# Kernel optimization log

Hardware: AMD Instinct MI355X
Metric: run time of the kernel (lower is better)

The kernel has to match this reference:

```python
import jax, jax.numpy as jnp
import numpy as np

B, T, C, H = 2, 2048, 1024, 16
HD = C // H  # head dim = 64


def setup_inputs() -> dict:
    key = jax.random.key(0)
    ks = jax.random.split(key, 5)
    s = 1.0 / np.sqrt(C)
    return {
        "x": jax.random.normal(ks[0], (B, T, C), dtype=jnp.float32),
        "Wq": jax.random.normal(ks[1], (C, C), dtype=jnp.float32) * s,
        "bq": jnp.zeros((C,), dtype=jnp.float32),
        "Wk": jax.random.normal(ks[2], (C, C), dtype=jnp.float32) * s,
        "bk": jnp.zeros((C,), dtype=jnp.float32),
        "Wv": jax.random.normal(ks[3], (C, C), dtype=jnp.float32) * s,
        "bv": jnp.zeros((C,), dtype=jnp.float32),
        "Wp": jax.random.normal(ks[4], (C, C), dtype=jnp.float32) * s,
        "bp": jnp.zeros((C,), dtype=jnp.float32),
    }


def reference(x, Wq, bq, Wk, bk, Wv, bv, Wp, bp):
    # QKV projections -> [B, H, T, HD]
    def proj(W, b):
        return (x @ W.T + b).reshape(B, T, H, HD).transpose(0, 2, 1, 3)

    q = proj(Wq, bq)
    k = proj(Wk, bk)
    v = proj(Wv, bv)

    scale = 1.0 / np.sqrt(HD)
    att = jnp.einsum("bhtd,bhsd->bhts", q, k) * scale  # [B,H,T,T]
    causal = jnp.tril(jnp.ones((T, T), dtype=bool))
    att = jnp.where(causal, att, -jnp.inf)
    att = jax.nn.softmax(att, axis=-1)
    y = jnp.einsum("bhts,bhsd->bhtd", att, v)          # [B,H,T,HD]
    y = y.transpose(0, 2, 1, 3).reshape(B, T, C)
    return y @ Wp.T + bp
```

## Files before the change

### kernel.cpp

```cpp
#include <hip/hip_runtime.h>
#include <hip/hip_bf16.h>

#define BB 2
#define TT 2048
#define CC 1024
#define HH 16
#define HDD 64

typedef __attribute__((ext_vector_type(8))) short bf16x8;
typedef __attribute__((ext_vector_type(4))) float f32x4;

static __device__ __forceinline__ unsigned short f2bf(float f) {
  union { float f; unsigned u; } v; v.f = f;
  unsigned r = v.u + 0x7fffu + ((v.u >> 16) & 1u);
  return (unsigned short)(r >> 16);
}

static __device__ __forceinline__ unsigned fbits(float f) {
  union { float f; unsigned u; } v; v.f = f; return v.u;
}

static __device__ __forceinline__ unsigned pk_trunc(float lo, float hi) {
  return __builtin_amdgcn_perm(fbits(hi), fbits(lo), 0x07060302u);
}

static __device__ __forceinline__ void gload_lds16(const unsigned short* g, unsigned short* l) {
  __builtin_amdgcn_global_load_lds((const __attribute__((address_space(1))) void*)g,
                                   (__attribute__((address_space(3))) void*)l, 16, 0, 0);
}

__global__ __launch_bounds__(256) void convert_all(
    const float* __restrict__ x, const float* __restrict__ Wq,
    const float* __restrict__ Wk, const float* __restrict__ Wv,
    const float* __restrict__ Wp, unsigned short* __restrict__ dst)
{
  const size_t M4 = 4194304, M1 = 1048576;
  const size_t e = ((size_t)blockIdx.x * 256 + threadIdx.x) * 8;
  const float* src; size_t off;
  if (e < M4)            { src = x;  off = e; }
  else if (e < M4 + M1)  { src = Wq; off = e - M4; }
  else if (e < M4 + 2*M1){ src = Wk; off = e - M4 - M1; }
  else if (e < M4 + 3*M1){ src = Wv; off = e - M4 - 2*M1; }
  else                   { src = Wp; off = e - M4 - 3*M1; }
  float4 a = *(const float4*)(src + off);
  float4 c = *(const float4*)(src + off + 4);
  unsigned short buf[8] = {f2bf(a.x), f2bf(a.y), f2bf(a.z), f2bf(a.w),
                           f2bf(c.x), f2bf(c.y), f2bf(c.z), f2bf(c.w)};
  *(uint4*)(dst + e) = *(const uint4*)buf;
}

__global__ __launch_bounds__(256) void gemm_mfma(
    const unsigned short* __restrict__ A, const unsigned short* __restrict__ W,
    const float* __restrict__ b0, const float* __restrict__ b1, const float* __restrict__ b2,
    unsigned short* __restrict__ oQ, unsigned short* __restrict__ oK,
    unsigned short* __restrict__ oVt)
{
  __shared__ unsigned short As[128][32];
  __shared__ unsigned short Bs[128][32];
  const int t = threadIdx.x;
  const int wv = __builtin_amdgcn_readfirstlane(t >> 6);
  const int ln = t & 63;
  const int l16 = ln & 15;
  const int quad = ln >> 4;
  const int mBase = blockIdx.x * 128;
  const int nBase = blockIdx.y * 128;
  const int wm = (wv >> 1) * 64, wn = (wv & 1) * 64;

  f32x4 acc[4][4];
#pragma unroll
  for (int i = 0; i < 4; i++)
#pragma unroll
    for (int j = 0; j < 4; j++) acc[i][j] = (f32x4){0.f, 0.f, 0.f, 0.f};

  const int ca = wv * 64 + ln;
  const int cb = ca + 256;
  const int ra = ca >> 2, colA = (ca & 3) * 8;
  const int rb = cb >> 2, colB = (cb & 3) * 8;
  unsigned short* ldsA0 = &As[0][0] + (size_t)(wv * 64) * 8;
  unsigned short* ldsA1 = &As[0][0] + (size_t)(256 + wv * 64) * 8;
  unsigned short* ldsB0 = &Bs[0][0] + (size_t)(wv * 64) * 8;
  unsigned short* ldsB1 = &Bs[0][0] + (size_t)(256 + wv * 64) * 8;
  const unsigned short* apA0 = A + (size_t)(mBase + ra) * CC + colA;
  const unsigned short* apA1 = A + (size_t)(mBase + rb) * CC + colB;
  const unsigned short* apB0 = W + (size_t)(nBase + ra) * CC + colA;
  const unsigned short* apB1 = W + (size_t)(nBase + rb) * CC + colB;

  for (int kb = 0; kb < CC; kb += 32) {
    __syncthreads();
    gload_lds16(apA0 + kb, ldsA0);
    gload_lds16(apA1 + kb, ldsA1);
    gload_lds16(apB0 + kb, ldsB0);
    gload_lds16(apB1 + kb, ldsB1);
    __syncthreads();
    bf16x8 af[4], bfr[4];
#pragma unroll
    for (int i = 0; i < 4; i++) af[i] = *(const bf16x8*)&As[wm + i * 16 + l16][quad * 8];
#pragma unroll
    for (int j = 0; j < 4; j++) bfr[j] = *(const bf16x8*)&Bs[wn + j * 16 + l16][quad * 8];
#pragma unroll
    for (int i = 0; i < 4; i++)
#pragma unroll
      for (int j = 0; j < 4; j++)
        acc[i][j] = __builtin_amdgcn_mfma_f32_16x16x32_bf16(af[i], bfr[j], acc[i][j], 0, 0, 0);
  }

  const int which = nBase >> 10;
  const float* bias = which == 0 ? b0 : (which == 1 ? b1 : b2);
  unsigned short* dst = which == 0 ? oQ : (which == 1 ? oK : oVt);
  const float scl = which == 0 ? 0.1803368801f : 1.0f;
#pragma unroll
  for (int i = 0; i < 4; i++)
#pragma unroll
    for (int r = 0; r < 4; r++) {
      const int m = mBase + wm + i * 16 + quad * 4 + r;
      const int b = m >> 11, tp = m & 2047;
#pragma unroll
      for (int j = 0; j < 4; j++) {
        const int n = nBase + wn + j * 16 + l16;
        const int nl = n & 1023, h = nl >> 6, d = nl & 63;
        const unsigned short v = f2bf((acc[i][j][r] + bias[nl]) * scl);
        if (which < 2) dst[((size_t)(b * HH + h) * TT + tp) * HDD + d] = v;
        else           dst[((size_t)(b * HH + h) * HDD + d) * TT + tp] = v;
      }
    }
}

__global__ __launch_bounds__(512) void gemm_proj(
    const unsigned short* __restrict__ A, const unsigned short* __restrict__ W,
    const float* __restrict__ bias, float* __restrict__ out)
{
  __shared__ unsigned short As[128][32];
  __shared__ unsigned short Bs[128][32];
  const int t = threadIdx.x;
  const int wv = __builtin_amdgcn_readfirstlane(t >> 6);
  const int ln = t & 63;
  const int l16 = ln & 15;
  const int quad = ln >> 4;
  const int mBase = blockIdx.x * 128;
  const int nBase = blockIdx.y * 128;
  const int wm = (wv >> 2) * 64;
  const int wn = (wv & 3) * 32;

  f32x4 acc[4][2];
#pragma unroll
  for (int i = 0; i < 4; i++)
#pragma unroll
    for (int j = 0; j < 2; j++) acc[i][j] = (f32x4){0.f, 0.f, 0.f, 0.f};

  const int rs = t >> 2, cs = (t & 3) * 8;
  unsigned short* ldsA = &As[0][0] + (size_t)t * 8;
  unsigned short* ldsB = &Bs[0][0] + (size_t)t * 8;
  const unsigned short* apA = A + (size_t)(mBase + rs) * CC + cs;
  const unsigned short* apB = W + (size_t)(nBase + rs) * CC + cs;

  for (int kb = 0; kb < CC; kb += 32) {
    __syncthreads();
    gload_lds16(apA + kb, ldsA);
    gload_lds16(apB + kb, ldsB);
    __syncthreads();
    bf16x8 af[4], bfr[2];
#pragma unroll
    for (int i = 0; i < 4; i++) af[i] = *(const bf16x8*)&As[wm + i * 16 + l16][quad * 8];
#pragma unroll
    for (int j = 0; j < 2; j++) bfr[j] = *(const bf16x8*)&Bs[wn + j * 16 + l16][quad * 8];
#pragma unroll
    for (int i = 0; i < 4; i++)
#pragma unroll
      for (int j = 0; j < 2; j++)
        acc[i][j] = __builtin_amdgcn_mfma_f32_16x16x32_bf16(af[i], bfr[j], acc[i][j], 0, 0, 0);
  }

#pragma unroll
  for (int i = 0; i < 4; i++)
#pragma unroll
    for (int r = 0; r < 4; r++) {
      const int m = mBase + wm + i * 16 + quad * 4 + r;
#pragma unroll
      for (int j = 0; j < 2; j++) {
        const int n = nBase + wn + j * 16 + l16;
        out[(size_t)m * CC + n] = acc[i][j][r] + bias[n];
      }
    }
}

__global__ __launch_bounds__(256, 2) void attn_mfma(
    const unsigned short* __restrict__ Q, const unsigned short* __restrict__ K,
    const unsigned short* __restrict__ Vt, unsigned short* __restrict__ y)
{
  __shared__ unsigned short QP[128][72];
  __shared__ unsigned short Ks[2][64][72];
  __shared__ unsigned short Vts[2][64][72];

  const int t = threadIdx.x;
  const int a = blockIdx.x;
  const int bh = blockIdx.y;
  const int wave = t >> 6;
  const int lane = t & 63;
  const int l16 = lane & 15;
  const int quad = lane >> 4;

  const size_t base = (size_t)bh * TT * HDD;
  const int qtL = a, qtH = 31 - a;
  const int qBaseL = qtL * 64, qBaseH = qtH * 64;

#pragma unroll
  for (int p = 0; p < 4; p++) {
    const int c = p * 256 + t;
    const int r = c >> 3, off = (c & 7) * 8;
    const int srcRow = (r < 64) ? (qBaseL + r) : (qBaseH + r - 64);
    *(uint4*)&QP[r][off] = *(const uint4*)(Q + base + (size_t)srcRow * HDD + off);
  }

  const int sr = t >> 2, sc = (t & 3) * 8;
  const unsigned short* kbase = K + base + (size_t)sr * HDD + sc;
  const unsigned short* vbase = Vt + base + (size_t)sr * TT + sc;
  uint4 kr0 = *(const uint4*)(kbase);
  uint4 kr1 = *(const uint4*)(kbase + 32);
  uint4 vr0 = *(const uint4*)(vbase);
  uint4 vr1 = *(const uint4*)(vbase + 32);
  __syncthreads();

  bf16x8 qfL0 = *(const bf16x8*)&QP[wave * 16 + l16][quad * 8];
  bf16x8 qfL1 = *(const bf16x8*)&QP[wave * 16 + l16][32 + quad * 8];
  bf16x8 qfH0 = *(const bf16x8*)&QP[64 + wave * 16 + l16][quad * 8];
  bf16x8 qfH1 = *(const bf16x8*)&QP[64 + wave * 16 + l16][32 + quad * 8];
  unsigned short (*PtH)[72] = (unsigned short (*)[72])&QP[wave * 16];
  unsigned short (*PtL)[72] = (unsigned short (*)[72])&QP[64 + wave * 16];

  float lL = 0.f, lH = 0.f;
  f32x4 OfrL[4], OfrH[4];
#pragma unroll
  for (int dt = 0; dt < 4; dt++) {
    OfrL[dt] = (f32x4){0.f, 0.f, 0.f, 0.f};
    OfrH[dt] = (f32x4){0.f, 0.f, 0.f, 0.f};
  }

  for (int kt = 0; kt <= qtH; kt++) {
    const int buf = kt & 1;
    *(uint4*)&Ks[buf][sr][sc]       = kr0;
    *(uint4*)&Ks[buf][sr][sc + 32]  = kr1;
    *(uint4*)&Vts[buf][sr][sc]      = vr0;
    *(uint4*)&Vts[buf][sr][sc + 32] = vr1;
    __syncthreads();
    if (kt < qtH) {
      kr0 = *(const uint4*)(kbase + (size_t)(kt + 1) * 64 * HDD);
      kr1 = *(const uint4*)(kbase + (size_t)(kt + 1) * 64 * HDD + 32);
      vr0 = *(const uint4*)(vbase + (kt + 1) * 64);
      vr1 = *(const uint4*)(vbase + (kt + 1) * 64 + 32);
    }
    const bool doLo = (kt <= qtL);

    f32x4 StH[4], StL[4];
#pragma unroll
    for (int ct = 0; ct < 4; ct++) {
      bf16x8 a0 = *(const bf16x8*)&Ks[buf][ct * 16 + l16][quad * 8];
      bf16x8 a1 = *(const bf16x8*)&Ks[buf][ct * 16 + l16][32 + quad * 8];
      f32x4 s = (f32x4){0.f, 0.f, 0.f, 0.f};
      s = __builtin_amdgcn_mfma_f32_16x16x32_bf16(a0, qfH0, s, 0, 0, 0);
      s = __builtin_amdgcn_mfma_f32_16x16x32_bf16(a1, qfH1, s, 0, 0, 0);
      StH[ct] = s;
      if (doLo) {
        f32x4 s2 = (f32x4){0.f, 0.f, 0.f, 0.f};
        s2 = __builtin_amdgcn_mfma_f32_16x16x32_bf16(a0, qfL0, s2, 0, 0, 0);
        s2 = __builtin_amdgcn_mfma_f32_16x16x32_bf16(a1, qfL1, s2, 0, 0, 0);
        StL[ct] = s2;
      }
    }

    if (kt == qtH) {
#pragma unroll
      for (int ct = 0; ct < 4; ct++) {
        float p[4];
#pragma unroll
        for (int r = 0; r < 4; r++) {
          float pv = exp2f(StH[ct][r]);
          if (ct * 16 + quad * 4 + r > wave * 16 + l16) pv = 0.f;
          lH += pv;
          p[r] = pv;
        }
        uint2 pk = {pk_trunc(p[0], p[1]), pk_trunc(p[2], p[3])};
        *(uint2*)&PtH[l16][ct * 16 + quad * 4] = pk;
      }
    } else {
#pragma unroll
      for (int ct = 0; ct < 4; ct++) {
        float p[4];
#pragma unroll
        for (int r = 0; r < 4; r++) {
          const float pv = exp2f(StH[ct][r]);
          lH += pv;
          p[r] = pv;
        }
        uint2 pk = {pk_trunc(p[0], p[1]), pk_trunc(p[2], p[3])};
        *(uint2*)&PtH[l16][ct * 16 + quad * 4] = pk;
      }
    }
    if (doLo) {
      if (kt == qtL) {
#pragma unroll
        for (int ct = 0; ct < 4; ct++) {
          float p[4];
#pragma unroll
          for (int r = 0; r < 4; r++) {
            float pv = exp2f(StL[ct][r]);
            if (ct * 16 + quad * 4 + r > wave * 16 + l16) pv = 0.f;
            lL += pv;
            p[r] = pv;
          }
          uint2 pk = {pk_trunc(p[0], p[1]), pk_trunc(p[2], p[3])};
          *(uint2*)&PtL[l16][ct * 16 + quad * 4] = pk;
        }
      } else {
#pragma unroll
        for (int ct = 0; ct < 4; ct++) {
          float p[4];
#pragma unroll
          for (int r = 0; r < 4; r++) {
            const float pv = exp2f(StL[ct][r]);
            lL += pv;
            p[r] = pv;
          }
          uint2 pk = {pk_trunc(p[0], p[1]), pk_trunc(p[2], p[3])};
          *(uint2*)&PtL[l16][ct * 16 + quad * 4] = pk;
        }
      }
    }

    bf16x8 paH0 = *(const bf16x8*)&PtH[l16][quad * 8];
    bf16x8 paH1 = *(const bf16x8*)&PtH[l16][32 + quad * 8];
    bf16x8 paL0, paL1;
    if (doLo) {
      paL0 = *(const bf16x8*)&PtL[l16][quad * 8];
      paL1 = *(const bf16x8*)&PtL[l16][32 + quad * 8];
    }
#pragma unroll
    for (int dt = 0; dt < 4; dt++) {
      bf16x8 vb0 = *(const bf16x8*)&Vts[buf][dt * 16 + l16][quad * 8];
      bf16x8 vb1 = *(const bf16x8*)&Vts[buf][dt * 16 + l16][32 + quad * 8];
      OfrH[dt] = __builtin_amdgcn_mfma_f32_16x16x32_bf16(paH0, vb0, OfrH[dt], 0, 0, 0);
      OfrH[dt] = __builtin_amdgcn_mfma_f32_16x16x32_bf16(paH1, vb1, OfrH[dt], 0, 0, 0);
      if (doLo) {
        OfrL[dt] = __builtin_amdgcn_mfma_f32_16x16x32_bf16(paL0, vb0, OfrL[dt], 0, 0, 0);
        OfrL[dt] = __builtin_amdgcn_mfma_f32_16x16x32_bf16(paL1, vb1, OfrL[dt], 0, 0, 0);
      }
    }
  }

  lL += __shfl_xor(lL, 16, 64); lL += __shfl_xor(lL, 32, 64);
  lH += __shfl_xor(lH, 16, 64); lH += __shfl_xor(lH, 32, 64);

  const int b = bh >> 4, h = bh & 15;
  float lRowL[4], lRowH[4];
#pragma unroll
  for (int r = 0; r < 4; r++) {
    lRowL[r] = __shfl(lL, quad * 4 + r, 16);
    lRowH[r] = __shfl(lH, quad * 4 + r, 16);
  }
#pragma unroll
  for (int r = 0; r < 4; r++) {
    const int qL = qBaseL + wave * 16 + quad * 4 + r;
    const int qH = qBaseH + wave * 16 + quad * 4 + r;
    const float invL = 1.0f / lRowL[r];
    const float invH = 1.0f / lRowH[r];
    unsigned short* ypL = y + ((size_t)(b * TT + qL)) * CC + h * 64 + l16;
    unsigned short* ypH = y + ((size_t)(b * TT + qH)) * CC + h * 64 + l16;
#pragma unroll
    for (int dt = 0; dt < 4; dt++) {
      ypL[dt * 16] = f2bf(OfrL[dt][r] * invL);
      ypH[dt * 16] = f2bf(OfrH[dt][r] * invH);
    }
  }
}

extern "C" void kernel_launch(void* const* d_in, const int* in_sizes, int n_in,
                              void* d_out, int out_size, void* d_ws, size_t ws_size,
                              hipStream_t stream) {
  const float* x  = (const float*)d_in[0];
  const float* Wq = (const float*)d_in[1];
  const float* bq = (const float*)d_in[2];
  const float* Wk = (const float*)d_in[3];
  const float* bk = (const float*)d_in[4];
  const float* Wv = (const float*)d_in[5];
  const float* bv = (const float*)d_in[6];
  const float* Wp = (const float*)d_in[7];
  const float* bp = (const float*)d_in[8];

  const size_t M4 = 4194304, M1 = 1048576;
  unsigned short* xb   = (unsigned short*)d_ws;
  unsigned short* wqb  = xb + M4;
  unsigned short* wpb  = wqb + 3 * M1;
  unsigned short* wsQ  = wpb + M1;
  unsigned short* wsK  = wsQ + M4;
  unsigned short* wsVt = wsK + M4;
  unsigned short* yb   = wsVt + M4;

  convert_all<<<4096, 256, 0, stream>>>(x, Wq, Wk, Wv, Wp, xb);
  gemm_mfma<<<dim3(32, 24), 256, 0, stream>>>(xb, wqb, bq, bk, bv,
                                              wsQ, wsK, wsVt);
  attn_mfma<<<dim3(16, BB * HH), 256, 0, stream>>>(wsQ, wsK, wsVt, yb);
  gemm_proj<<<dim3(32, 8), 512, 0, stream>>>(yb, wpb, bp, (float*)d_out);
}
```

Measured before the change: 188.1 us.

## Split paired causal query tiles into one tile per block, heaviest first

The attention kernel no longer pairs a light and a heavy query tile per block. Each block now processes one 64-row query tile, launched in reverse order so long causal rows start first, and the grid doubles. Q fragments are loaded straight from global memory, and the P scratch buffer moves to a dedicated per-wave LDS array. This cuts LDS use and raises the occupancy target to 3 blocks per CU, at the cost of no longer sharing each K/V tile load between two query tiles.

```diff
diff --git a/kernel.cpp b/kernel.cpp
--- a/kernel.cpp
+++ b/kernel.cpp
@@ -183,16 +183,16 @@
     }
 }
 
-__global__ __launch_bounds__(256, 2) void attn_mfma(
+__global__ __launch_bounds__(256, 3) void attn_mfma(
     const unsigned short* __restrict__ Q, const unsigned short* __restrict__ K,
     const unsigned short* __restrict__ Vt, unsigned short* __restrict__ y)
 {
-  __shared__ unsigned short QP[128][72];
   __shared__ unsigned short Ks[2][64][72];
   __shared__ unsigned short Vts[2][64][72];
+  __shared__ unsigned short Pt[4][16][72];
 
   const int t = threadIdx.x;
-  const int a = blockIdx.x;
+  const int qt = 31 - blockIdx.x;
   const int bh = blockIdx.y;
   const int wave = t >> 6;
   const int lane = t & 63;
@@ -200,16 +200,11 @@
   const int quad = lane >> 4;
 
   const size_t base = (size_t)bh * TT * HDD;
-  const int qtL = a, qtH = 31 - a;
-  const int qBaseL = qtL * 64, qBaseH = qtH * 64;
-
-#pragma unroll
-  for (int p = 0; p < 4; p++) {
-    const int c = p * 256 + t;
-    const int r = c >> 3, off = (c & 7) * 8;
-    const int srcRow = (r < 64) ? (qBaseL + r) : (qBaseH + r - 64);
-    *(uint4*)&QP[r][off] = *(const uint4*)(Q + base + (size_t)srcRow * HDD + off);
-  }
+  const int qBase = qt * 64;
+
+  const unsigned short* qrow = Q + base + (size_t)(qBase + wave * 16 + l16) * HDD + quad * 8;
+  bf16x8 qf0 = *(const bf16x8*)(qrow);
+  bf16x8 qf1 = *(const bf16x8*)(qrow + 32);
 
   const int sr = t >> 2, sc = (t & 3) * 8;
   const unsigned short* kbase = K + base + (size_t)sr * HDD + sc;
@@ -218,68 +213,50 @@
   uint4 kr1 = *(const uint4*)(kbase + 32);
   uint4 vr0 = *(const uint4*)(vbase);
   uint4 vr1 = *(const uint4*)(vbase + 32);
-  __syncthreads();
-
-  bf16x8 qfL0 = *(const bf16x8*)&QP[wave * 16 + l16][quad * 8];
-  bf16x8 qfL1 = *(const bf16x8*)&QP[wave * 16 + l16][32 + quad * 8];
-  bf16x8 qfH0 = *(const bf16x8*)&QP[64 + wave * 16 + l16][quad * 8];
-  bf16x8 qfH1 = *(const bf16x8*)&QP[64 + wave * 16 + l16][32 + quad * 8];
-  unsigned short (*PtH)[72] = (unsigned short (*)[72])&QP[wave * 16];
-  unsigned short (*PtL)[72] = (unsigned short (*)[72])&QP[64 + wave * 16];
-
-  float lL = 0.f, lH = 0.f;
-  f32x4 OfrL[4], OfrH[4];
-#pragma unroll
-  for (int dt = 0; dt < 4; dt++) {
-    OfrL[dt] = (f32x4){0.f, 0.f, 0.f, 0.f};
-    OfrH[dt] = (f32x4){0.f, 0.f, 0.f, 0.f};
-  }
-
-  for (int kt = 0; kt <= qtH; kt++) {
+
+  float lsum = 0.f;
+  f32x4 Ofr[4];
+#pragma unroll
+  for (int dt = 0; dt < 4; dt++) Ofr[dt] = (f32x4){0.f, 0.f, 0.f, 0.f};
+
+  for (int kt = 0; kt <= qt; kt++) {
     const int buf = kt & 1;
     *(uint4*)&Ks[buf][sr][sc]       = kr0;
     *(uint4*)&Ks[buf][sr][sc + 32]  = kr1;
     *(uint4*)&Vts[buf][sr][sc]      = vr0;
     *(uint4*)&Vts[buf][sr][sc + 32] = vr1;
     __syncthreads();
-    if (kt < qtH) {
+    if (kt < qt) {
       kr0 = *(const uint4*)(kbase + (size_t)(kt + 1) * 64 * HDD);
       kr1 = *(const uint4*)(kbase + (size_t)(kt + 1) * 64 * HDD + 32);
       vr0 = *(const uint4*)(vbase + (kt + 1) * 64);
       vr1 = *(const uint4*)(vbase + (kt + 1) * 64 + 32);
     }
-    const bool doLo = (kt <= qtL);
-
-    f32x4 StH[4], StL[4];
+
+    f32x4 St[4];
 #pragma unroll
     for (int ct = 0; ct < 4; ct++) {
       bf16x8 a0 = *(const bf16x8*)&Ks[buf][ct * 16 + l16][quad * 8];
       bf16x8 a1 = *(const bf16x8*)&Ks[buf][ct * 16 + l16][32 + quad * 8];
       f32x4 s = (f32x4){0.f, 0.f, 0.f, 0.f};
-      s = __builtin_amdgcn_mfma_f32_16x16x32_bf16(a0, qfH0, s, 0, 0, 0);
-      s = __builtin_amdgcn_mfma_f32_16x16x32_bf16(a1, qfH1, s, 0, 0, 0);
-      StH[ct] = s;
-      if (doLo) {
-        f32x4 s2 = (f32x4){0.f, 0.f, 0.f, 0.f};
-        s2 = __builtin_amdgcn_mfma_f32_16x16x32_bf16(a0, qfL0, s2, 0, 0, 0);
-        s2 = __builtin_amdgcn_mfma_f32_16x16x32_bf16(a1, qfL1, s2, 0, 0, 0);
-        StL[ct] = s2;
-      }
-    }
-
-    if (kt == qtH) {
+      s = __builtin_amdgcn_mfma_f32_16x16x32_bf16(a0, qf0, s, 0, 0, 0);
+      s = __builtin_amdgcn_mfma_f32_16x16x32_bf16(a1, qf1, s, 0, 0, 0);
+      St[ct] = s;
+    }
+
+    if (kt == qt) {
 #pragma unroll
       for (int ct = 0; ct < 4; ct++) {
         float p[4];
 #pragma unroll
         for (int r = 0; r < 4; r++) {
-          float pv = exp2f(StH[ct][r]);
+          float pv = exp2f(St[ct][r]);
           if (ct * 16 + quad * 4 + r > wave * 16 + l16) pv = 0.f;
-          lH += pv;
+          lsum += pv;
           p[r] = pv;
         }
         uint2 pk = {pk_trunc(p[0], p[1]), pk_trunc(p[2], p[3])};
-        *(uint2*)&PtH[l16][ct * 16 + quad * 4] = pk;
+        *(uint2*)&Pt[wave][l16][ct * 16 + quad * 4] = pk;
       }
     } else {
 #pragma unroll
@@ -287,88 +264,40 @@
         float p[4];
 #pragma unroll
         for (int r = 0; r < 4; r++) {
-          const float pv = exp2f(StH[ct][r]);
-          lH += pv;
+          const float pv = exp2f(St[ct][r]);
+          lsum += pv;
           p[r] = pv;
         }
         uint2 pk = {pk_trunc(p[0], p[1]), pk_trunc(p[2], p[3])};
-        *(uint2*)&PtH[l16][ct * 16 + quad * 4] = pk;
+        *(uint2*)&Pt[wave][l16][ct * 16 + quad * 4] = pk;
       }
     }
-    if (doLo) {
-      if (kt == qtL) {
-#pragma unroll
-        for (int ct = 0; ct < 4; ct++) {
-          float p[4];
-#pragma unroll
-          for (int r = 0; r < 4; r++) {
-            float pv = exp2f(StL[ct][r]);
-            if (ct * 16 + quad * 4 + r > wave * 16 + l16) pv = 0.f;
-            lL += pv;
-            p[r] = pv;
-          }
-          uint2 pk = {pk_trunc(p[0], p[1]), pk_trunc(p[2], p[3])};
-          *(uint2*)&PtL[l16][ct * 16 + quad * 4] = pk;
-        }
-      } else {
-#pragma unroll
-        for (int ct = 0; ct < 4; ct++) {
-          float p[4];
-#pragma unroll
-          for (int r = 0; r < 4; r++) {
-            const float pv = exp2f(StL[ct][r]);
-            lL += pv;
-            p[r] = pv;
-          }
-          uint2 pk = {pk_trunc(p[0], p[1]), pk_trunc(p[2], p[3])};
-          *(uint2*)&PtL[l16][ct * 16 + quad * 4] = pk;
-        }
-      }
-    }
-
-    bf16x8 paH0 = *(const bf16x8*)&PtH[l16][quad * 8];
-    bf16x8 paH1 = *(const bf16x8*)&PtH[l16][32 + quad * 8];
-    bf16x8 paL0, paL1;
-    if (doLo) {
-      paL0 = *(const bf16x8*)&PtL[l16][quad * 8];
-      paL1 = *(const bf16x8*)&PtL[l16][32 + quad * 8];
-    }
+
+    bf16x8 pa0 = *(const bf16x8*)&Pt[wave][l16][quad * 8];
+    bf16x8 pa1 = *(const bf16x8*)&Pt[wave][l16][32 + quad * 8];
 #pragma unroll
     for (int dt = 0; dt < 4; dt++) {
       bf16x8 vb0 = *(const bf16x8*)&Vts[buf][dt * 16 + l16][quad * 8];
       bf16x8 vb1 = *(const bf16x8*)&Vts[buf][dt * 16 + l16][32 + quad * 8];
-      OfrH[dt] = __builtin_amdgcn_mfma_f32_16x16x32_bf16(paH0, vb0, OfrH[dt], 0, 0, 0);
-      OfrH[dt] = __builtin_amdgcn_mfma_f32_16x16x32_bf16(paH1, vb1, OfrH[dt], 0, 0, 0);
-      if (doLo) {
-        OfrL[dt] = __builtin_amdgcn_mfma_f32_16x16x32_bf16(paL0, vb0, OfrL[dt], 0, 0, 0);
-        OfrL[dt] = __builtin_amdgcn_mfma_f32_16x16x32_bf16(paL1, vb1, OfrL[dt], 0, 0, 0);
-      }
+      Ofr[dt] = __builtin_amdgcn_mfma_f32_16x16x32_bf16(pa0, vb0, Ofr[dt], 0, 0, 0);
+      Ofr[dt] = __builtin_amdgcn_mfma_f32_16x16x32_bf16(pa1, vb1, Ofr[dt], 0, 0, 0);
     }
   }
 
-  lL += __shfl_xor(lL, 16, 64); lL += __shfl_xor(lL, 32, 64);
-  lH += __shfl_xor(lH, 16, 64); lH += __shfl_xor(lH, 32, 64);
+  lsum += __shfl_xor(lsum, 16, 64);
+  lsum += __shfl_xor(lsum, 32, 64);
 
   const int b = bh >> 4, h = bh & 15;
-  float lRowL[4], lRowH[4];
+  float lRow[4];
+#pragma unroll
+  for (int r = 0; r < 4; r++) lRow[r] = __shfl(lsum, quad * 4 + r, 16);
 #pragma unroll
   for (int r = 0; r < 4; r++) {
-    lRowL[r] = __shfl(lL, quad * 4 + r, 16);
-    lRowH[r] = __shfl(lH, quad * 4 + r, 16);
-  }
-#pragma unroll
-  for (int r = 0; r < 4; r++) {
-    const int qL = qBaseL + wave * 16 + quad * 4 + r;
-    const int qH = qBaseH + wave * 16 + quad * 4 + r;
-    const float invL = 1.0f / lRowL[r];
-    const float invH = 1.0f / lRowH[r];
-    unsigned short* ypL = y + ((size_t)(b * TT + qL)) * CC + h * 64 + l16;
-    unsigned short* ypH = y + ((size_t)(b * TT + qH)) * CC + h * 64 + l16;
-#pragma unroll
-    for (int dt = 0; dt < 4; dt++) {
-      ypL[dt * 16] = f2bf(OfrL[dt][r] * invL);
-      ypH[dt * 16] = f2bf(OfrH[dt][r] * invH);
-    }
+    const int q = qBase + wave * 16 + quad * 4 + r;
+    const float inv = 1.0f / lRow[r];
+    unsigned short* yp = y + ((size_t)(b * TT + q)) * CC + h * 64 + l16;
+#pragma unroll
+    for (int dt = 0; dt < 4; dt++) yp[dt * 16] = f2bf(Ofr[dt][r] * inv);
   }
 }
 
@@ -397,6 +326,6 @@
   convert_all<<<4096, 256, 0, stream>>>(x, Wq, Wk, Wv, Wp, xb);
   gemm_mfma<<<dim3(32, 24), 256, 0, stream>>>(xb, wqb, bq, bk, bv,
                                               wsQ, wsK, wsVt);
-  attn_mfma<<<dim3(16, BB * HH), 256, 0, stream>>>(wsQ, wsK, wsVt, yb);
+  attn_mfma<<<dim3(32, BB * HH), 256, 0, stream>>>(wsQ, wsK, wsVt, yb);
   gemm_proj<<<dim3(32, 8), 512, 0, stream>>>(yb, wpb, bp, (float*)d_out);
 }
```

Measured after the change: 213.6 us. +13.6%, slower.
